# Optimization experiments

Measured on AMD Instinct MI355X. Metric: run time of the kernel, lower is better.

## Reference

```python
import jax, jax.numpy as jnp
import numpy as np

B = 1024      # num graphs
NPG = 128     # nodes per graph
N = B * NPG
EPG = 512     # edges per graph
E = B * EPG
D = 64
MAX_STEPS = 4
S = MAX_STEPS + 1   # max_steps + stop-step offset
T = 1.0
TB = 1.0
NEG = -1e30
STOP = -1


def setup_inputs() -> dict:
    key = jax.random.key(0)
    ks = jax.random.split(key, 24)
    edge_batch = jnp.repeat(jnp.arange(B, dtype=jnp.int32), EPG)
    src = jax.random.randint(ks[0], (E,), 0, NPG, dtype=jnp.int32) + edge_batch * NPG
    dst = jax.random.randint(ks[1], (E,), 0, NPG, dtype=jnp.int32) + edge_batch * NPG
    edge_index = jnp.stack([src, dst])
    sc = 1.0 / np.sqrt(D)
    p = lambda k, shape: (jax.random.normal(k, shape, jnp.float32) * sc)
    return dict(
        node_tokens=p(ks[2], (N, D)), edge_emb=p(ks[3], (E, D)),
        Wf1=p(ks[4], (D, D)), Wnf=p(ks[5], (D, D)), Wf2=p(ks[6], (D, D)),
        bf=jnp.zeros((D,), jnp.float32), wf=p(ks[7], (D,)),
        Wb1=p(ks[8], (D, D)), Wnb=p(ks[9], (D, D)), Wb2=p(ks[10], (D, D)),
        bb=jnp.zeros((D,), jnp.float32), wb=p(ks[11], (D,)),
        w_stop=p(ks[12], (D,)), b_stop=jnp.zeros((), jnp.float32),
        Ws=p(ks[13], (D, D)), Wu=p(ks[14], (D, D)), bu=jnp.zeros((D,), jnp.float32),
        edge_index=edge_index, edge_batch=edge_batch,
    )


def reference(node_tokens, edge_emb, Wf1, Wnf, Wf2, bf, wf,
              Wb1, Wnb, Wb2, bb, wb, w_stop, b_stop, Ws, Wu, bu,
              edge_index, edge_batch):
    esrc, edst = edge_index[0], edge_index[1]
    # state-independent part of the edge scores (precomputed once; faithful math)
    base_f = edge_emb @ Wf1 + node_tokens[esrc] @ Wnf + bf   # [E,D]
    base_b = edge_emb @ Wb1 + node_tokens[edst] @ Wnb + bb   # [E,D]
    g_ids = jnp.arange(B, dtype=jnp.int32)
    eidx = jnp.arange(E, dtype=jnp.int32)

    def seg_lse(x, valid):
        # per-graph logsumexp over valid edges (grad-safe masking)
        xm = jnp.where(valid, x, NEG)
        m = jax.ops.segment_max(xm, edge_batch, num_segments=B)
        xc = jnp.where(valid, x - m[edge_batch], 0.0)
        s = jax.ops.segment_sum(jnp.where(valid, jnp.exp(xc), 0.0), edge_batch, num_segments=B)
        return m + jnp.log(jnp.maximum(s, 1e-30))

    def step_fn(carry, k):
        state_vec, active, used, done, steps, stopn = carry
        valid = (esrc == active[edge_batch]) & (~used) & (~done[edge_batch])
        allow_stop = (~done) & (steps < MAX_STEPS)
        # forward edge scores + stop logit
        h = jax.nn.relu(base_f + (state_vec @ Wf2)[edge_batch])   # [E,D]
        score = h @ wf                                            # [E]
        stop_logit = state_vec @ w_stop + b_stop                  # [B]
        x = score / T
        lse_e = seg_lse(x, valid)
        stop_t = jnp.where(allow_stop, stop_logit / T, NEG)
        Z = jnp.logaddexp(lse_e, stop_t)
        logp_edge = x - Z[edge_batch]
        logp_stop = jnp.where(allow_stop, stop_logit / T - Z, 0.0)
        has_edge = jax.ops.segment_sum(valid.astype(jnp.int32), edge_batch, num_segments=B) > 0
        # gumbel-max sampling with scatter_max semantics
        ke, ksn = jax.random.split(k)
        se = jnp.where(valid, logp_edge + jax.random.gumbel(ke, (E,)), NEG)
        ss = jnp.where(allow_stop, logp_stop + jax.random.gumbel(ksn, (B,)), NEG)
        m = jax.ops.segment_max(se, edge_batch, num_segments=B)
        amax = jax.ops.segment_min(jnp.where(se == m[edge_batch], eidx, E), edge_batch, num_segments=B)
        amax = jnp.where(has_edge, amax, 0).astype(jnp.int32)
        m = jnp.where(has_edge, m, NEG)
        choose_stop = (ss > m) | (~has_edge)
        actions = jnp.where(choose_stop | done, STOP, amax)
        log_pf = jnp.where(choose_stop, logp_stop, logp_edge[amax])
        log_pf = jnp.where(done, 0.0, log_pf)
        take_edge = (actions >= 0) & (~done)
        stopping = choose_stop & (~done)
        stopn = jnp.where((stopn < 0) & stopping, active - g_ids * NPG, stopn)
        # state encoder update (masked)
        rel = edge_emb[amax]                                      # [B,D]
        new_state = jnp.tanh(state_vec @ Ws + rel @ Wu + bu)
        state_vec = jnp.where(take_edge[:, None], new_state, state_vec)
        # env step
        new_active = jnp.where(take_edge, edst[amax], active)
        used = used.at[amax].max(take_edge)
        steps = steps + take_edge.astype(jnp.int32)
        new_done = done | stopping
        # backward policy log-prob over edges incoming to the new active node
        bvalid = edst == new_active[edge_batch]
        hb = jax.nn.relu(base_b + (state_vec @ Wb2)[edge_batch])
        xb = (hb @ wb) / TB
        lse_b = seg_lse(xb, bvalid)
        log_pb = jnp.where(take_edge, xb[amax] - lse_b, 0.0)
        return (state_vec, new_active, used, new_done, steps, stopn), (actions, log_pf, log_pb)

    init = (
        jnp.zeros((B, D), jnp.float32),      # state_vec
        g_ids * NPG,                          # active node (global) = graph start node
        jnp.zeros((E,), bool),                # used_edge_mask
        jnp.zeros((B,), bool),                # done
        jnp.zeros((B,), jnp.int32),           # step_counts
        jnp.full((B,), STOP, jnp.int32),      # stop_node_locals
    )
    keys = jax.random.split(jax.random.key(42), S)
    (state_vec, active, used, done, steps, stopn), ys = jax.lax.scan(step_fn, init, keys)
    actions_seq = ys[0].T      # [B,S]
    log_pf_steps = ys[1].T     # [B,S]
    log_pb_steps = ys[2].T     # [B,S]
    stopn = jnp.where(stopn < 0, active - g_ids * NPG, stopn)   # backfill stop nodes
    return (actions_seq, log_pf_steps.sum(1), log_pf_steps, log_pb_steps,
            used, stopn, steps.astype(jnp.float32))
```

## Files before the change

kernel.cpp:

```cpp
#include <hip/hip_runtime.h>
#include <hip/hip_bf16.h>
#include <cstdint>

#define NBLK 1024
#define NPG  128
#define EPG  512
#define DD   64
#define NSTEP 5
#define ETOT (NBLK*EPG)
#define NEGF (-1e30f)
#define WAVES 4
#define MAXDEG 32

#define OA  0
#define OLS 5120
#define OPF 6144
#define OPB 11264
#define OU  16384
#define OSN 540672
#define OST 541696

struct KeysArg {
  uint32_t ke0[NSTEP], ke1[NSTEP];
  uint32_t ks0[NSTEP], ks1[NSTEP];
};

__host__ __device__ inline uint32_t rotl32(uint32_t x, int r){ return (x<<r)|(x>>(32-r)); }

__host__ __device__ inline void tf2x32(uint32_t k0, uint32_t k1, uint32_t& x0, uint32_t& x1){
  uint32_t k2 = k0 ^ k1 ^ 0x1BD11BDAu;
  x0 += k0; x1 += k1;
  x0+=x1; x1=rotl32(x1,13); x1^=x0;
  x0+=x1; x1=rotl32(x1,15); x1^=x0;
  x0+=x1; x1=rotl32(x1,26); x1^=x0;
  x0+=x1; x1=rotl32(x1, 6); x1^=x0;
  x0+=k1; x1+=k2+1u;
  x0+=x1; x1=rotl32(x1,17); x1^=x0;
  x0+=x1; x1=rotl32(x1,29); x1^=x0;
  x0+=x1; x1=rotl32(x1,16); x1^=x0;
  x0+=x1; x1=rotl32(x1,24); x1^=x0;
  x0+=k2; x1+=k0+2u;
  x0+=x1; x1=rotl32(x1,13); x1^=x0;
  x0+=x1; x1=rotl32(x1,15); x1^=x0;
  x0+=x1; x1=rotl32(x1,26); x1^=x0;
  x0+=x1; x1=rotl32(x1, 6); x1^=x0;
  x0+=k0; x1+=k1+3u;
  x0+=x1; x1=rotl32(x1,17); x1^=x0;
  x0+=x1; x1=rotl32(x1,29); x1^=x0;
  x0+=x1; x1=rotl32(x1,16); x1^=x0;
  x0+=x1; x1=rotl32(x1,24); x1^=x0;
  x0+=k1; x1+=k2+4u;
  x0+=x1; x1=rotl32(x1,13); x1^=x0;
  x0+=x1; x1=rotl32(x1,15); x1^=x0;
  x0+=x1; x1=rotl32(x1,26); x1^=x0;
  x0+=x1; x1=rotl32(x1, 6); x1^=x0;
  x0+=k2; x1+=k0+5u;
}

__device__ inline float gumbel_from_bits(uint32_t bits){
  float f = __uint_as_float((bits>>9) | 0x3f800000u) - 1.0f;
  const float tiny = 1.17549435e-38f;
  float u = fmaxf(tiny, f * (1.0f - tiny) + tiny);
  return -logf(-logf(u));
}

__device__ inline float gumbel_part(uint32_t k0, uint32_t k1, uint32_t idx){
  uint32_t x0 = 0u, x1 = idx;
  tf2x32(k0, k1, x0, x1);
  return gumbel_from_bits(x0 ^ x1);
}

__device__ inline float wsum(float x){
  #pragma unroll
  for (int off = 32; off; off >>= 1) x += __shfl_xor(x, off, 64);
  return x;
}

__device__ __forceinline__ void wsum4(float& x0, float& x1, float& x2, float& x3){
  #pragma unroll
  for (int off = 32; off; off >>= 1){
    x0 += __shfl_xor(x0, off, 64);
    x1 += __shfl_xor(x1, off, 64);
    x2 += __shfl_xor(x2, off, 64);
    x3 += __shfl_xor(x3, off, 64);
  }
}

__device__ __forceinline__ float rdlane(float v, int i){
  return __int_as_float(__builtin_amdgcn_readlane(__float_as_int(v), i));
}
__device__ __forceinline__ int rdlane_i(int v, int i){
  return __builtin_amdgcn_readlane(v, i);
}

__device__ __forceinline__ float matvec_col(const float* __restrict__ W, float v, int lane){
  float a0=0.f, a1=0.f, a2=0.f, a3=0.f;
  #pragma unroll 4
  for (int i = 0; i < DD; i += 4){
    a0 = fmaf(rdlane(v, i  ), W[(i  )*DD+lane], a0);
    a1 = fmaf(rdlane(v, i+1), W[(i+1)*DD+lane], a1);
    a2 = fmaf(rdlane(v, i+2), W[(i+2)*DD+lane], a2);
    a3 = fmaf(rdlane(v, i+3), W[(i+3)*DD+lane], a3);
  }
  return (a0+a1)+(a2+a3);
}

__device__ __forceinline__ void matvec4(const float* __restrict__ W,
                                        float v0, float v1, float v2, float v3,
                                        int lane, float o[4]){
  float acc[4][4] = {{0,0,0,0},{0,0,0,0},{0,0,0,0},{0,0,0,0}};
  #pragma unroll 8
  for (int i = 0; i < DD; i += 4){
    #pragma unroll
    for (int t = 0; t < 4; t++){
      float w  = W[(i+t)*DD+lane];
      acc[0][t] = fmaf(rdlane(v0, i+t), w, acc[0][t]);
      acc[1][t] = fmaf(rdlane(v1, i+t), w, acc[1][t]);
      acc[2][t] = fmaf(rdlane(v2, i+t), w, acc[2][t]);
      acc[3][t] = fmaf(rdlane(v3, i+t), w, acc[3][t]);
    }
  }
  #pragma unroll
  for (int c = 0; c < 4; c++)
    o[c] = (acc[c][0]+acc[c][1])+(acc[c][2]+acc[c][3]);
}

__global__ void __launch_bounds__(256, 4)
gfn_fused(const float* __restrict__ node_tokens,
          const float* __restrict__ edge_emb,
          const float* __restrict__ Wf1, const float* __restrict__ Wnf, const float* __restrict__ Wf2,
          const float* __restrict__ bf,  const float* __restrict__ wf,
          const float* __restrict__ Wb1, const float* __restrict__ Wnb, const float* __restrict__ Wb2,
          const float* __restrict__ bb,  const float* __restrict__ wb,
          const float* __restrict__ w_stop, const float* __restrict__ b_stop,
          const float* __restrict__ Ws,  const float* __restrict__ Wu, const float* __restrict__ bu,
          const int* __restrict__ e_src, const int* __restrict__ e_dst,
          float* __restrict__ out, KeysArg keys)
{
  const int g    = blockIdx.x;
  const int tid  = threadIdx.x;
  const int lane = tid & 63;
  const int wave = tid >> 6;
  const int ebase = g * EPG;

  __shared__ uint8_t  srcL[EPG], dstL[EPG];
  __shared__ uint16_t listO[EPG], listI[EPG];
  __shared__ int cntO[NPG], cntI[NPG], begO[NPG], begI[NPG];
  __shared__ uint8_t usedL[EPG];
  __shared__ float st_sh[DD];
  __shared__ float u_sh[DD], nt_sh[DD], acs_sh[DD];
  __shared__ float ntb_sh[DD], ntN_sh[DD], uN_sh[DD], ubB_sh[DD];
  __shared__ float xcF[MAXDEG], gmF[MAXDEG], xcB[MAXDEG];
  __shared__ float sl_sh, xbb_sh;

  for (int j = tid; j < EPG; j += 256){
    srcL[j] = (uint8_t)(e_src[ebase+j] - g*NPG);
    dstL[j] = (uint8_t)(e_dst[ebase+j] - g*NPG);
    usedL[j] = 0;
  }
  for (int n = tid; n < NPG; n += 256){ cntO[n]=0; cntI[n]=0; }
  if (tid < DD) st_sh[tid] = 0.f;
  __syncthreads();

  for (int j = tid; j < EPG; j += 256){
    atomicAdd(&cntO[srcL[j]], 1);
    atomicAdd(&cntI[dstL[j]], 1);
  }
  __syncthreads();

  if (wave == 0){
    int n0 = lane*2, n1 = n0+1;
    int c0O=cntO[n0], c1O=cntO[n1], sO=c0O+c1O;
    int c0I=cntI[n0], c1I=cntI[n1], sI=c0I+c1I;
    int xO=sO, xI=sI;
    #pragma unroll
    for (int off=1; off<64; off<<=1){
      int tO=__shfl_up(xO,off,64), tI=__shfl_up(xI,off,64);
      if (lane>=off){ xO+=tO; xI+=tI; }
    }
    begO[n0]=xO-sO; begO[n1]=xO-c1O;
    begI[n0]=xI-sI; begI[n1]=xI-c1I;
  }
  __syncthreads();
  for (int n = tid; n < NPG; n += 256){ cntO[n]=0; cntI[n]=0; }
  __syncthreads();

  for (int ph = 0; ph < WAVES; ph++){
    if (wave == ph){
      #pragma unroll
      for (int h = 0; h < 2; h++){
        int j = ph*128 + h*64 + lane;
        int sL = srcL[j]; int p = atomicAdd(&cntO[sL],1); listO[begO[sL]+p] = (uint16_t)j;
        int dL = dstL[j]; int q = atomicAdd(&cntI[dL],1); listI[begI[dL]+q] = (uint16_t)j;
      }
    }
    __syncthreads();
  }

  const float bf_l = bf[lane], wf_l = wf[lane];
  const float bb_l = bb[lane], wb_l = wb[lane];
  const float bu_l = bu[lane], wst_l = w_stop[lane];
  const float bstop = b_stop[0];

  bool done = false;
  int stepsC = 0, stopn = -1, activeL = 0;
  float lpf_sum = 0.f;
  int bOF = begO[0], dOF = min(cntO[0], MAXDEG);

  {
    float st_v = st_sh[lane];
    if (wave == 0)      u_sh[lane]   = matvec_col(Wf2, st_v, lane);
    else if (wave == 1){ float ntv = node_tokens[(size_t)(g*NPG+0)*DD+lane];
                         nt_sh[lane] = matvec_col(Wnf, ntv, lane); }
    else if (wave == 2) acs_sh[lane] = matvec_col(Ws, st_v, lane);
    else {
      float sl = wsum(st_v * wst_l) + bstop;
      if (lane == 0) sl_sh = sl;
      if (lane < dOF)
        gmF[lane] = gumbel_part(keys.ke0[0], keys.ke1[0], (uint32_t)(ebase + listO[bOF+lane]));
    }
    __syncthreads();
    if (wave >= 2){
      for (int c = wave-2; c < (dOF+3)>>2; c += 2){
        int el[4]; float v[4];
        #pragma unroll
        for (int t = 0; t < 4; t++){
          int k = c*4 + t;
          el[t] = listO[bOF + min(k, dOF-1)];
          v[t]  = edge_emb[(size_t)(ebase+el[t])*DD + lane];
        }
        float o[4], x[4];
        matvec4(Wf1, v[0], v[1], v[2], v[3], lane, o);
        #pragma unroll
        for (int t = 0; t < 4; t++) x[t] = fmaxf(o[t] + nt_sh[lane] + bf_l + u_sh[lane], 0.f) * wf_l;
        wsum4(x[0], x[1], x[2], x[3]);
        #pragma unroll
        for (int t = 0; t < 4; t++){
          int k = c*4 + t;
          if (k < dOF && lane == 0) xcF[k] = usedL[el[t]] ? NEGF : x[t];
        }
      }
    }
    __syncthreads();
  }

  for (int s = 0; s < NSTEP; s++){
    float act_out = -1.f, lpf_out = 0.f, lpb_out = 0.f;
    if (!done){
      float xr = (lane < MAXDEG) ? xcF[lane] : NEGF;
      float gr = (lane < MAXDEG) ? gmF[lane] : 0.f;
      int   er = (lane < dOF)    ? (int)listO[bOF + lane] : -1;
      float sl = sl_sh;

      float m1 = NEGF; int nvalid = 0;
      for (int k=0;k<dOF;k++){ float xk=rdlane(xr,k); if (xk!=NEGF){ m1=fmaxf(m1,xk); nvalid++; } }
      float ssum = 0.f;
      for (int k=0;k<dOF;k++){ float xk=rdlane(xr,k); if (xk!=NEGF) ssum += expf(xk - m1); }
      const bool has_edge = nvalid > 0;
      float lse_e = m1 + logf(fmaxf(ssum, 1e-30f));
      const bool allow_stop = (stepsC < 4);
      float stop_t = allow_stop ? sl : NEGF;
      float amx = fmaxf(lse_e, stop_t);
      float Z = amx + log1pf(expf(-fabsf(lse_e - stop_t)));

      float mbest = NEGF; int elbest = -1; float xbest = 0.f;
      for (int k=0;k<dOF;k++){
        float xk = rdlane(xr,k);
        if (xk == NEGF) continue;
        float se = (xk - Z) + rdlane(gr,k);
        if (se > mbest){ mbest = se; elbest = rdlane_i(er,k); xbest = xk; }
      }
      float gs = gumbel_part(keys.ks0[s], keys.ks1[s], (uint32_t)g);
      float ss = allow_stop ? (sl - Z) + gs : NEGF;
      float mcmp = has_edge ? mbest : NEGF;
      const bool choose_stop = (ss > mcmp) || (!has_edge);
      float logp_stop = allow_stop ? (sl - Z) : 0.f;
      const bool take_edge = !choose_stop;

      act_out = choose_stop ? -1.f : (float)(ebase + elbest);
      lpf_out = choose_stop ? logp_stop : (xbest - Z);
      if (choose_stop && stopn < 0) stopn = activeL;

      if (take_edge){
        const int newA = dstL[elbest];
        const bool more = (s < NSTEP-1);

        if (wave == 0){
          float rv = edge_emb[(size_t)(ebase+elbest)*DD + lane];
          float acr = matvec_col(Wu, rv, lane);
          st_sh[lane] = tanhf(acs_sh[lane] + acr + bu_l);
          if (lane == 0) usedL[elbest] = 1;
        } else if (wave == 1){
          float nbv = node_tokens[(size_t)(g*NPG + newA)*DD + lane];
          ntb_sh[lane] = matvec_col(Wnb, nbv, lane);
        } else if (wave == 2){
          if (more){
            float nbv = node_tokens[(size_t)(g*NPG + newA)*DD + lane];
            ntN_sh[lane] = matvec_col(Wnf, nbv, lane);
          }
        }
        activeL = newA; stepsC++;
        __syncthreads();

        float stp = st_sh[lane];
        const int bI  = begI[activeL], dIc = min(cntI[activeL], MAXDEG);
        const int bON = begO[activeL];
        const int dON = more ? min(cntO[activeL], MAXDEG) : 0;
        if (wave == 0){
          if (more) uN_sh[lane] = matvec_col(Wf2, stp, lane);
        } else if (wave == 1){
          ubB_sh[lane] = matvec_col(Wb2, stp, lane);
        } else if (wave == 2){
          if (more) acs_sh[lane] = matvec_col(Ws, stp, lane);
        } else {
          if (more){
            float s2 = wsum(stp * wst_l) + bstop;
            if (lane == 0) sl_sh = s2;
            if (lane < dON)
              gmF[lane] = gumbel_part(keys.ke0[s+1], keys.ke1[s+1],
                                      (uint32_t)(ebase + listO[bON+lane]));
          }
        }
        __syncthreads();

        if (wave == 2 || wave == 0){
          for (int c = (wave==2 ? 0 : 1); c < (dIc+3)>>2; c += 2){
            int el[4]; float v[4];
            #pragma unroll
            for (int t = 0; t < 4; t++){
              int k = c*4 + t;
              el[t] = listI[bI + min(k, dIc-1)];
              v[t]  = edge_emb[(size_t)(ebase+el[t])*DD + lane];
            }
            float o[4], xb[4];
            matvec4(Wb1, v[0], v[1], v[2], v[3], lane, o);
            #pragma unroll
            for (int t = 0; t < 4; t++) xb[t] = fmaxf(o[t] + ntb_sh[lane] + bb_l + ubB_sh[lane], 0.f) * wb_l;
            wsum4(xb[0], xb[1], xb[2], xb[3]);
            #pragma unroll
            for (int t = 0; t < 4; t++){
              int k = c*4 + t;
              if (k < dIc && lane == 0){
                xcB[k] = xb[t];
                if (el[t] == elbest) xbb_sh = xb[t];
              }
            }
          }
        } else {
          for (int c = (wave==3 ? 0 : 1); c < (dON+3)>>2; c += 2){
            int el[4]; float v[4];
            #pragma unroll
            for (int t = 0; t < 4; t++){
              int k = c*4 + t;
              el[t] = listO[bON + min(k, dON-1)];
              v[t]  = edge_emb[(size_t)(ebase+el[t])*DD + lane];
            }
            float o[4], x[4];
            matvec4(Wf1, v[0], v[1], v[2], v[3], lane, o);
            #pragma unroll
            for (int t = 0; t < 4; t++) x[t] = fmaxf(o[t] + ntN_sh[lane] + bf_l + uN_sh[lane], 0.f) * wf_l;
            wsum4(x[0], x[1], x[2], x[3]);
            #pragma unroll
            for (int t = 0; t < 4; t++){
              int k = c*4 + t;
              if (k < dON && lane == 0) xcF[k] = usedL[el[t]] ? NEGF : x[t];
            }
          }
        }
        __syncthreads();

        float xbr = (lane < MAXDEG) ? xcB[lane] : 0.f;
        float m2 = NEGF;
        for (int k=0;k<dIc;k++) m2 = fmaxf(m2, rdlane(xbr,k));
        float s2 = 0.f;
        for (int k=0;k<dIc;k++) s2 += expf(rdlane(xbr,k) - m2);
        float lse_b = m2 + logf(fmaxf(s2, 1e-30f));
        lpb_out = xbb_sh - lse_b;

        bOF = bON; dOF = dON;
      }
      done = done || choose_stop;
    }

    if (tid == 0){
      out[OA  + g*NSTEP + s] = act_out;
      out[OPF + g*NSTEP + s] = lpf_out;
      out[OPB + g*NSTEP + s] = lpb_out;
    }
    lpf_sum += lpf_out;
  }

  if (tid == 0){
    out[OLS + g] = lpf_sum;
    int sn = (stopn < 0) ? activeL : stopn;
    out[OSN + g] = (float)sn;
    out[OST + g] = (float)stepsC;
  }
  for (int j = tid; j < EPG; j += 256)
    out[OU + ebase + j] = usedL[j] ? 1.0f : 0.0f;
}

extern "C" void kernel_launch(void* const* d_in, const int* in_sizes, int n_in,
                              void* d_out, int out_size, void* d_ws, size_t ws_size,
                              hipStream_t stream)
{
  (void)in_sizes; (void)n_in; (void)out_size; (void)d_ws; (void)ws_size;

  KeysArg K;
  for (uint32_t s = 0; s < NSTEP; s++){
    uint32_t a = 0u, b = s;
    tf2x32(0u, 42u, a, b);
    uint32_t e0 = 0u, e1 = 0u;
    tf2x32(a, b, e0, e1);
    uint32_t s0 = 0u, s1 = 1u;
    tf2x32(a, b, s0, s1);
    K.ke0[s] = e0; K.ke1[s] = e1;
    K.ks0[s] = s0; K.ks1[s] = s1;
  }

  const int* eidx = (const int*)d_in[17];
  gfn_fused<<<dim3(NBLK), dim3(256), 0, stream>>>(
      (const float*)d_in[0],  (const float*)d_in[1],
      (const float*)d_in[2],  (const float*)d_in[3],  (const float*)d_in[4],
      (const float*)d_in[5],  (const float*)d_in[6],
      (const float*)d_in[7],  (const float*)d_in[8],  (const float*)d_in[9],
      (const float*)d_in[10], (const float*)d_in[11],
      (const float*)d_in[12], (const float*)d_in[13],
      (const float*)d_in[14], (const float*)d_in[15], (const float*)d_in[16],
      eidx, eidx + ETOT,
      (float*)d_out, K);
}
```

Before: 81.07 us.

## Pack four graphs per block and stage six weight matrices in LDS

Each block now holds four 256-thread teams, one per graph. The six DxD weight matrices (Wf1, Wb1, Wnf, Wnb, Wf2, Wb2) are loaded once into shared memory and shared by all teams, so matvecs read LDS instead of global/L2. Barriers are hoisted out of divergent branches so all 1024 threads synchronise together. The trade-off is that teams now wait on each other at every barrier, and about 96KB of LDS per block limits occupancy to roughly one block per CU. The launch grid also shrinks to 256 blocks.

```diff
diff --git a/kernel.cpp b/kernel.cpp
--- a/kernel.cpp
+++ b/kernel.cpp
@@ -10,6 +10,7 @@
 #define ETOT (NBLK*EPG)
 #define NEGF (-1e30f)
 #define WAVES 4
+#define TEAMS 4
 #define MAXDEG 32
 
 #define OA  0
@@ -125,7 +126,7 @@
     o[c] = (acc[c][0]+acc[c][1])+(acc[c][2]+acc[c][3]);
 }
 
-__global__ void __launch_bounds__(256, 4)
+__global__ void __launch_bounds__(1024)
 gfn_fused(const float* __restrict__ node_tokens,
           const float* __restrict__ edge_emb,
           const float* __restrict__ Wf1, const float* __restrict__ Wnf, const float* __restrict__ Wf2,
@@ -137,52 +138,62 @@
           const int* __restrict__ e_src, const int* __restrict__ e_dst,
           float* __restrict__ out, KeysArg keys)
 {
-  const int g    = blockIdx.x;
   const int tid  = threadIdx.x;
+  const int team = tid >> 8;
+  const int ttid = tid & 255;
   const int lane = tid & 63;
-  const int wave = tid >> 6;
+  const int wave = (tid >> 6) & 3;
+  const int g    = blockIdx.x * TEAMS + team;
   const int ebase = g * EPG;
 
-  __shared__ uint8_t  srcL[EPG], dstL[EPG];
-  __shared__ uint16_t listO[EPG], listI[EPG];
-  __shared__ int cntO[NPG], cntI[NPG], begO[NPG], begI[NPG];
-  __shared__ uint8_t usedL[EPG];
-  __shared__ float st_sh[DD];
-  __shared__ float u_sh[DD], nt_sh[DD], acs_sh[DD];
-  __shared__ float ntb_sh[DD], ntN_sh[DD], uN_sh[DD], ubB_sh[DD];
-  __shared__ float xcF[MAXDEG], gmF[MAXDEG], xcB[MAXDEG];
-  __shared__ float sl_sh, xbb_sh;
-
-  for (int j = tid; j < EPG; j += 256){
-    srcL[j] = (uint8_t)(e_src[ebase+j] - g*NPG);
-    dstL[j] = (uint8_t)(e_dst[ebase+j] - g*NPG);
-    usedL[j] = 0;
-  }
-  for (int n = tid; n < NPG; n += 256){ cntO[n]=0; cntI[n]=0; }
-  if (tid < DD) st_sh[tid] = 0.f;
+  __shared__ float Wlds[6][DD*DD];
+  __shared__ uint8_t  srcL[TEAMS][EPG], dstL[TEAMS][EPG];
+  __shared__ uint16_t listO[TEAMS][EPG], listI[TEAMS][EPG];
+  __shared__ int cntO[TEAMS][NPG], cntI[TEAMS][NPG], begO[TEAMS][NPG], begI[TEAMS][NPG];
+  __shared__ uint8_t usedL[TEAMS][EPG];
+  __shared__ float st_sh[TEAMS][DD];
+  __shared__ float u_sh[TEAMS][DD], nt_sh[TEAMS][DD], acs_sh[TEAMS][DD];
+  __shared__ float ntb_sh[TEAMS][DD], ntN_sh[TEAMS][DD], uN_sh[TEAMS][DD], ubB_sh[TEAMS][DD];
+  __shared__ float xcF[TEAMS][MAXDEG], gmF[TEAMS][MAXDEG], xcB[TEAMS][MAXDEG];
+  __shared__ float sl_sh[TEAMS], xbb_sh[TEAMS];
+
+  {
+    const float* srcs[6] = {Wf1, Wb1, Wnf, Wnb, Wf2, Wb2};
+    #pragma unroll
+    for (int m = 0; m < 6; m++)
+      ((float4*)&Wlds[m][0])[tid] = ((const float4*)srcs[m])[tid];
+  }
+
+  for (int j = ttid; j < EPG; j += 256){
+    srcL[team][j] = (uint8_t)(e_src[ebase+j] - g*NPG);
+    dstL[team][j] = (uint8_t)(e_dst[ebase+j] - g*NPG);
+    usedL[team][j] = 0;
+  }
+  for (int n = ttid; n < NPG; n += 256){ cntO[team][n]=0; cntI[team][n]=0; }
+  if (ttid < DD) st_sh[team][ttid] = 0.f;
   __syncthreads();
 
-  for (int j = tid; j < EPG; j += 256){
-    atomicAdd(&cntO[srcL[j]], 1);
-    atomicAdd(&cntI[dstL[j]], 1);
+  for (int j = ttid; j < EPG; j += 256){
+    atomicAdd(&cntO[team][srcL[team][j]], 1);
+    atomicAdd(&cntI[team][dstL[team][j]], 1);
   }
   __syncthreads();
 
   if (wave == 0){
     int n0 = lane*2, n1 = n0+1;
-    int c0O=cntO[n0], c1O=cntO[n1], sO=c0O+c1O;
-    int c0I=cntI[n0], c1I=cntI[n1], sI=c0I+c1I;
+    int c0O=cntO[team][n0], c1O=cntO[team][n1], sO=c0O+c1O;
+    int c0I=cntI[team][n0], c1I=cntI[team][n1], sI=c0I+c1I;
     int xO=sO, xI=sI;
     #pragma unroll
     for (int off=1; off<64; off<<=1){
       int tO=__shfl_up(xO,off,64), tI=__shfl_up(xI,off,64);
       if (lane>=off){ xO+=tO; xI+=tI; }
     }
-    begO[n0]=xO-sO; begO[n1]=xO-c1O;
-    begI[n0]=xI-sI; begI[n1]=xI-c1I;
+    begO[team][n0]=xO-sO; begO[team][n1]=xO-c1O;
+    begI[team][n0]=xI-sI; begI[team][n1]=xI-c1I;
   }
   __syncthreads();
-  for (int n = tid; n < NPG; n += 256){ cntO[n]=0; cntI[n]=0; }
+  for (int n = ttid; n < NPG; n += 256){ cntO[team][n]=0; cntI[team][n]=0; }
   __syncthreads();
 
   for (int ph = 0; ph < WAVES; ph++){
@@ -190,8 +201,8 @@
       #pragma unroll
       for (int h = 0; h < 2; h++){
         int j = ph*128 + h*64 + lane;
-        int sL = srcL[j]; int p = atomicAdd(&cntO[sL],1); listO[begO[sL]+p] = (uint16_t)j;
-        int dL = dstL[j]; int q = atomicAdd(&cntI[dL],1); listI[begI[dL]+q] = (uint16_t)j;
+        int sL = srcL[team][j]; int p = atomicAdd(&cntO[team][sL],1); listO[team][begO[team][sL]+p] = (uint16_t)j;
+        int dL = dstL[team][j]; int q = atomicAdd(&cntI[team][dL],1); listI[team][begI[team][dL]+q] = (uint16_t)j;
       }
     }
     __syncthreads();
@@ -205,19 +216,19 @@
   bool done = false;
   int stepsC = 0, stopn = -1, activeL = 0;
   float lpf_sum = 0.f;
-  int bOF = begO[0], dOF = min(cntO[0], MAXDEG);
+  int bOF = begO[team][0], dOF = min(cntO[team][0], MAXDEG);
 
   {
-    float st_v = st_sh[lane];
-    if (wave == 0)      u_sh[lane]   = matvec_col(Wf2, st_v, lane);
+    float st_v = st_sh[team][lane];
+    if (wave == 0)      u_sh[team][lane]   = matvec_col(Wlds[4], st_v, lane);
     else if (wave == 1){ float ntv = node_tokens[(size_t)(g*NPG+0)*DD+lane];
-                         nt_sh[lane] = matvec_col(Wnf, ntv, lane); }
-    else if (wave == 2) acs_sh[lane] = matvec_col(Ws, st_v, lane);
+                         nt_sh[team][lane] = matvec_col(Wlds[2], ntv, lane); }
+    else if (wave == 2) acs_sh[team][lane] = matvec_col(Ws, st_v, lane);
     else {
       float sl = wsum(st_v * wst_l) + bstop;
-      if (lane == 0) sl_sh = sl;
+      if (lane == 0) sl_sh[team] = sl;
       if (lane < dOF)
-        gmF[lane] = gumbel_part(keys.ke0[0], keys.ke1[0], (uint32_t)(ebase + listO[bOF+lane]));
+        gmF[team][lane] = gumbel_part(keys.ke0[0], keys.ke1[0], (uint32_t)(ebase + listO[team][bOF+lane]));
     }
     __syncthreads();
     if (wave >= 2){
@@ -226,18 +237,18 @@
         #pragma unroll
         for (int t = 0; t < 4; t++){
           int k = c*4 + t;
-          el[t] = listO[bOF + min(k, dOF-1)];
+          el[t] = listO[team][bOF + min(k, dOF-1)];
           v[t]  = edge_emb[(size_t)(ebase+el[t])*DD + lane];
         }
         float o[4], x[4];
-        matvec4(Wf1, v[0], v[1], v[2], v[3], lane, o);
+        matvec4(Wlds[0], v[0], v[1], v[2], v[3], lane, o);
         #pragma unroll
-        for (int t = 0; t < 4; t++) x[t] = fmaxf(o[t] + nt_sh[lane] + bf_l + u_sh[lane], 0.f) * wf_l;
+        for (int t = 0; t < 4; t++) x[t] = fmaxf(o[t] + nt_sh[team][lane] + bf_l + u_sh[team][lane], 0.f) * wf_l;
         wsum4(x[0], x[1], x[2], x[3]);
         #pragma unroll
         for (int t = 0; t < 4; t++){
           int k = c*4 + t;
-          if (k < dOF && lane == 0) xcF[k] = usedL[el[t]] ? NEGF : x[t];
+          if (k < dOF && lane == 0) xcF[team][k] = usedL[team][el[t]] ? NEGF : x[t];
         }
       }
     }
@@ -246,11 +257,15 @@
 
   for (int s = 0; s < NSTEP; s++){
     float act_out = -1.f, lpf_out = 0.f, lpb_out = 0.f;
+    bool choose_stop = false, take_edge = false;
+    int elbest = -1, newA = 0, bI = 0, dIc = 0, bON = 0, dON = 0;
+    const bool more = (s < NSTEP-1);
+
     if (!done){
-      float xr = (lane < MAXDEG) ? xcF[lane] : NEGF;
-      float gr = (lane < MAXDEG) ? gmF[lane] : 0.f;
-      int   er = (lane < dOF)    ? (int)listO[bOF + lane] : -1;
-      float sl = sl_sh;
+      float xr = (lane < MAXDEG) ? xcF[team][lane] : NEGF;
+      float gr = (lane < MAXDEG) ? gmF[team][lane] : 0.f;
+      int   er = (lane < dOF)    ? (int)listO[team][bOF + lane] : -1;
+      float sl = sl_sh[team];
 
       float m1 = NEGF; int nvalid = 0;
       for (int k=0;k<dOF;k++){ float xk=rdlane(xr,k); if (xk!=NEGF){ m1=fmaxf(m1,xk); nvalid++; } }
@@ -263,7 +278,7 @@
       float amx = fmaxf(lse_e, stop_t);
       float Z = amx + log1pf(expf(-fabsf(lse_e - stop_t)));
 
-      float mbest = NEGF; int elbest = -1; float xbest = 0.f;
+      float mbest = NEGF; float xbest = 0.f;
       for (int k=0;k<dOF;k++){
         float xk = rdlane(xr,k);
         if (xk == NEGF) continue;
@@ -273,116 +288,119 @@
       float gs = gumbel_part(keys.ks0[s], keys.ks1[s], (uint32_t)g);
       float ss = allow_stop ? (sl - Z) + gs : NEGF;
       float mcmp = has_edge ? mbest : NEGF;
-      const bool choose_stop = (ss > mcmp) || (!has_edge);
+      choose_stop = (ss > mcmp) || (!has_edge);
       float logp_stop = allow_stop ? (sl - Z) : 0.f;
-      const bool take_edge = !choose_stop;
+      take_edge = !choose_stop;
 
       act_out = choose_stop ? -1.f : (float)(ebase + elbest);
       lpf_out = choose_stop ? logp_stop : (xbest - Z);
       if (choose_stop && stopn < 0) stopn = activeL;
-
-      if (take_edge){
-        const int newA = dstL[elbest];
-        const bool more = (s < NSTEP-1);
-
-        if (wave == 0){
-          float rv = edge_emb[(size_t)(ebase+elbest)*DD + lane];
-          float acr = matvec_col(Wu, rv, lane);
-          st_sh[lane] = tanhf(acs_sh[lane] + acr + bu_l);
-          if (lane == 0) usedL[elbest] = 1;
-        } else if (wave == 1){
+    }
+
+    if (take_edge){
+      newA = dstL[team][elbest];
+      if (wave == 0){
+        float rv = edge_emb[(size_t)(ebase+elbest)*DD + lane];
+        float acr = matvec_col(Wu, rv, lane);
+        st_sh[team][lane] = tanhf(acs_sh[team][lane] + acr + bu_l);
+        if (lane == 0) usedL[team][elbest] = 1;
+      } else if (wave == 1){
+        float nbv = node_tokens[(size_t)(g*NPG + newA)*DD + lane];
+        ntb_sh[team][lane] = matvec_col(Wlds[3], nbv, lane);
+      } else if (wave == 2){
+        if (more){
           float nbv = node_tokens[(size_t)(g*NPG + newA)*DD + lane];
-          ntb_sh[lane] = matvec_col(Wnb, nbv, lane);
-        } else if (wave == 2){
-          if (more){
-            float nbv = node_tokens[(size_t)(g*NPG + newA)*DD + lane];
-            ntN_sh[lane] = matvec_col(Wnf, nbv, lane);
+          ntN_sh[team][lane] = matvec_col(Wlds[2], nbv, lane);
+        }
+      }
+      activeL = newA; stepsC++;
+    }
+    __syncthreads();
+
+    if (take_edge){
+      float stp = st_sh[team][lane];
+      bI  = begI[team][activeL]; dIc = min(cntI[team][activeL], MAXDEG);
+      bON = begO[team][activeL];
+      dON = more ? min(cntO[team][activeL], MAXDEG) : 0;
+      if (wave == 0){
+        if (more) uN_sh[team][lane] = matvec_col(Wlds[4], stp, lane);
+      } else if (wave == 1){
+        ubB_sh[team][lane] = matvec_col(Wlds[5], stp, lane);
+      } else if (wave == 2){
+        if (more) acs_sh[team][lane] = matvec_col(Ws, stp, lane);
+      } else {
+        if (more){
+          float s2 = wsum(stp * wst_l) + bstop;
+          if (lane == 0) sl_sh[team] = s2;
+          if (lane < dON)
+            gmF[team][lane] = gumbel_part(keys.ke0[s+1], keys.ke1[s+1],
+                                          (uint32_t)(ebase + listO[team][bON+lane]));
+        }
+      }
+    }
+    __syncthreads();
+
+    if (take_edge){
+      if (wave == 2 || wave == 0){
+        for (int c = (wave==2 ? 0 : 1); c < (dIc+3)>>2; c += 2){
+          int el[4]; float v[4];
+          #pragma unroll
+          for (int t = 0; t < 4; t++){
+            int k = c*4 + t;
+            el[t] = listI[team][bI + min(k, dIc-1)];
+            v[t]  = edge_emb[(size_t)(ebase+el[t])*DD + lane];
           }
-        }
-        activeL = newA; stepsC++;
-        __syncthreads();
-
-        float stp = st_sh[lane];
-        const int bI  = begI[activeL], dIc = min(cntI[activeL], MAXDEG);
-        const int bON = begO[activeL];
-        const int dON = more ? min(cntO[activeL], MAXDEG) : 0;
-        if (wave == 0){
-          if (more) uN_sh[lane] = matvec_col(Wf2, stp, lane);
-        } else if (wave == 1){
-          ubB_sh[lane] = matvec_col(Wb2, stp, lane);
-        } else if (wave == 2){
-          if (more) acs_sh[lane] = matvec_col(Ws, stp, lane);
-        } else {
-          if (more){
-            float s2 = wsum(stp * wst_l) + bstop;
-            if (lane == 0) sl_sh = s2;
-            if (lane < dON)
-              gmF[lane] = gumbel_part(keys.ke0[s+1], keys.ke1[s+1],
-                                      (uint32_t)(ebase + listO[bON+lane]));
-          }
-        }
-        __syncthreads();
-
-        if (wave == 2 || wave == 0){
-          for (int c = (wave==2 ? 0 : 1); c < (dIc+3)>>2; c += 2){
-            int el[4]; float v[4];
-            #pragma unroll
-            for (int t = 0; t < 4; t++){
-              int k = c*4 + t;
-              el[t] = listI[bI + min(k, dIc-1)];
-              v[t]  = edge_emb[(size_t)(ebase+el[t])*DD + lane];
-            }
-            float o[4], xb[4];
-            matvec4(Wb1, v[0], v[1], v[2], v[3], lane, o);
-            #pragma unroll
-            for (int t = 0; t < 4; t++) xb[t] = fmaxf(o[t] + ntb_sh[lane] + bb_l + ubB_sh[lane], 0.f) * wb_l;
-            wsum4(xb[0], xb[1], xb[2], xb[3]);
-            #pragma unroll
-            for (int t = 0; t < 4; t++){
-              int k = c*4 + t;
-              if (k < dIc && lane == 0){
-                xcB[k] = xb[t];
-                if (el[t] == elbest) xbb_sh = xb[t];
-              }
+          float o[4], xb[4];
+          matvec4(Wlds[1], v[0], v[1], v[2], v[3], lane, o);
+          #pragma unroll
+          for (int t = 0; t < 4; t++) xb[t] = fmaxf(o[t] + ntb_sh[team][lane] + bb_l + ubB_sh[team][lane], 0.f) * wb_l;
+          wsum4(xb[0], xb[1], xb[2], xb[3]);
+          #pragma unroll
+          for (int t = 0; t < 4; t++){
+            int k = c*4 + t;
+            if (k < dIc && lane == 0){
+              xcB[team][k] = xb[t];
+              if (el[t] == elbest) xbb_sh[team] = xb[t];
             }
           }
-        } else {
-          for (int c = (wave==3 ? 0 : 1); c < (dON+3)>>2; c += 2){
-            int el[4]; float v[4];
-            #pragma unroll
-            for (int t = 0; t < 4; t++){
-              int k = c*4 + t;
-              el[t] = listO[bON + min(k, dON-1)];
-              v[t]  = edge_emb[(size_t)(ebase+el[t])*DD + lane];
-            }
-            float o[4], x[4];
-            matvec4(Wf1, v[0], v[1], v[2], v[3], lane, o);
-            #pragma unroll
-            for (int t = 0; t < 4; t++) x[t] = fmaxf(o[t] + ntN_sh[lane] + bf_l + uN_sh[lane], 0.f) * wf_l;
-            wsum4(x[0], x[1], x[2], x[3]);
-            #pragma unroll
-            for (int t = 0; t < 4; t++){
-              int k = c*4 + t;
-              if (k < dON && lane == 0) xcF[k] = usedL[el[t]] ? NEGF : x[t];
-            }
+        }
+      } else {
+        for (int c = (wave==3 ? 0 : 1); c < (dON+3)>>2; c += 2){
+          int el[4]; float v[4];
+          #pragma unroll
+          for (int t = 0; t < 4; t++){
+            int k = c*4 + t;
+            el[t] = listO[team][bON + min(k, dON-1)];
+            v[t]  = edge_emb[(size_t)(ebase+el[t])*DD + lane];
           }
-        }
-        __syncthreads();
-
-        float xbr = (lane < MAXDEG) ? xcB[lane] : 0.f;
-        float m2 = NEGF;
-        for (int k=0;k<dIc;k++) m2 = fmaxf(m2, rdlane(xbr,k));
-        float s2 = 0.f;
-        for (int k=0;k<dIc;k++) s2 += expf(rdlane(xbr,k) - m2);
-        float lse_b = m2 + logf(fmaxf(s2, 1e-30f));
-        lpb_out = xbb_sh - lse_b;
-
-        bOF = bON; dOF = dON;
-      }
-      done = done || choose_stop;
-    }
-
-    if (tid == 0){
+          float o[4], x[4];
+          matvec4(Wlds[0], v[0], v[1], v[2], v[3], lane, o);
+          #pragma unroll
+          for (int t = 0; t < 4; t++) x[t] = fmaxf(o[t] + ntN_sh[team][lane] + bf_l + uN_sh[team][lane], 0.f) * wf_l;
+          wsum4(x[0], x[1], x[2], x[3]);
+          #pragma unroll
+          for (int t = 0; t < 4; t++){
+            int k = c*4 + t;
+            if (k < dON && lane == 0) xcF[team][k] = usedL[team][el[t]] ? NEGF : x[t];
+          }
+        }
+      }
+    }
+    __syncthreads();
+
+    if (take_edge){
+      float xbr = (lane < MAXDEG) ? xcB[team][lane] : 0.f;
+      float m2 = NEGF;
+      for (int k=0;k<dIc;k++) m2 = fmaxf(m2, rdlane(xbr,k));
+      float s2 = 0.f;
+      for (int k=0;k<dIc;k++) s2 += expf(rdlane(xbr,k) - m2);
+      float lse_b = m2 + logf(fmaxf(s2, 1e-30f));
+      lpb_out = xbb_sh[team] - lse_b;
+      bOF = bON; dOF = dON;
+    }
+    done = done || choose_stop;
+
+    if (ttid == 0){
       out[OA  + g*NSTEP + s] = act_out;
       out[OPF + g*NSTEP + s] = lpf_out;
       out[OPB + g*NSTEP + s] = lpb_out;
@@ -390,14 +408,14 @@
     lpf_sum += lpf_out;
   }
 
-  if (tid == 0){
+  if (ttid == 0){
     out[OLS + g] = lpf_sum;
     int sn = (stopn < 0) ? activeL : stopn;
     out[OSN + g] = (float)sn;
     out[OST + g] = (float)stepsC;
   }
-  for (int j = tid; j < EPG; j += 256)
-    out[OU + ebase + j] = usedL[j] ? 1.0f : 0.0f;
+  for (int j = ttid; j < EPG; j += 256)
+    out[OU + ebase + j] = usedL[team][j] ? 1.0f : 0.0f;
 }
 
 extern "C" void kernel_launch(void* const* d_in, const int* in_sizes, int n_in,
@@ -419,7 +437,7 @@
   }
 
   const int* eidx = (const int*)d_in[17];
-  gfn_fused<<<dim3(NBLK), dim3(256), 0, stream>>>(
+  gfn_fused<<<dim3(NBLK/TEAMS), dim3(1024), 0, stream>>>(
       (const float*)d_in[0],  (const float*)d_in[1],
       (const float*)d_in[2],  (const float*)d_in[3],  (const float*)d_in[4],
       (const float*)d_in[5],  (const float*)d_in[6],
```

New measurement: 89.88 us. 10.9% more time.

## Prefetch first edge chunk early, vectorize softmax exps, precompute stop gumbels

Applied to the files above, without the earlier changes.

Moves the adjacency lookups for the new active node ahead of the state-update matvecs, so each wave can issue its first edge_emb gather early and hide global-memory latency behind the matvecs and barriers. Both per-edge exp loops now compute the exponentials once per lane and sum them with readlane, replacing serial scalar exps. The stop-action gumbel noise for all steps is precomputed once, one step per lane, instead of hashed each step. The matvec unroll factor also rises. Risks are higher register pressure from the held prefetch values and the larger unroll, which could lower occupancy.

```diff
diff --git a/kernel.cpp b/kernel.cpp
--- a/kernel.cpp
+++ b/kernel.cpp
@@ -95,7 +95,7 @@
 
 __device__ __forceinline__ float matvec_col(const float* __restrict__ W, float v, int lane){
   float a0=0.f, a1=0.f, a2=0.f, a3=0.f;
-  #pragma unroll 4
+  #pragma unroll 8
   for (int i = 0; i < DD; i += 4){
     a0 = fmaf(rdlane(v, i  ), W[(i  )*DD+lane], a0);
     a1 = fmaf(rdlane(v, i+1), W[(i+1)*DD+lane], a1);
@@ -202,6 +202,15 @@
   const float bu_l = bu[lane], wst_l = w_stop[lane];
   const float bstop = b_stop[0];
 
+  float gsv;
+  {
+    uint32_t k0 = keys.ks0[0], k1 = keys.ks1[0];
+    #pragma unroll
+    for (int s5 = 1; s5 < NSTEP; s5++)
+      if (lane == s5){ k0 = keys.ks0[s5]; k1 = keys.ks1[s5]; }
+    gsv = (lane < NSTEP) ? gumbel_part(k0, k1, (uint32_t)g) : 0.f;
+  }
+
   bool done = false;
   int stepsC = 0, stopn = -1, activeL = 0;
   float lpf_sum = 0.f;
@@ -254,8 +263,9 @@
 
       float m1 = NEGF; int nvalid = 0;
       for (int k=0;k<dOF;k++){ float xk=rdlane(xr,k); if (xk!=NEGF){ m1=fmaxf(m1,xk); nvalid++; } }
+      float ex = expf(xr - m1);
       float ssum = 0.f;
-      for (int k=0;k<dOF;k++){ float xk=rdlane(xr,k); if (xk!=NEGF) ssum += expf(xk - m1); }
+      for (int k=0;k<dOF;k++){ float xk=rdlane(xr,k); if (xk!=NEGF) ssum += rdlane(ex,k); }
       const bool has_edge = nvalid > 0;
       float lse_e = m1 + logf(fmaxf(ssum, 1e-30f));
       const bool allow_stop = (stepsC < 4);
@@ -270,7 +280,7 @@
         float se = (xk - Z) + rdlane(gr,k);
         if (se > mbest){ mbest = se; elbest = rdlane_i(er,k); xbest = xk; }
       }
-      float gs = gumbel_part(keys.ks0[s], keys.ks1[s], (uint32_t)g);
+      float gs = rdlane(gsv, s);
       float ss = allow_stop ? (sl - Z) + gs : NEGF;
       float mcmp = has_edge ? mbest : NEGF;
       const bool choose_stop = (ss > mcmp) || (!has_edge);
@@ -284,6 +294,34 @@
       if (take_edge){
         const int newA = dstL[elbest];
         const bool more = (s < NSTEP-1);
+        const int bI  = begI[newA], dIc = min(cntI[newA], MAXDEG);
+        const int bON = begO[newA];
+        const int dON = more ? min(cntO[newA], MAXDEG) : 0;
+
+        float vPre[4]; int elPre[4]; bool pre = false; int c0;
+        if (wave == 2 || wave == 0){
+          c0 = (wave==2 ? 0 : 1);
+          if (c0 < ((dIc+3)>>2)){
+            pre = true;
+            #pragma unroll
+            for (int t = 0; t < 4; t++){
+              int k = c0*4 + t;
+              elPre[t] = listI[bI + min(k, dIc-1)];
+              vPre[t]  = edge_emb[(size_t)(ebase+elPre[t])*DD + lane];
+            }
+          }
+        } else {
+          c0 = (wave==3 ? 0 : 1);
+          if (c0 < ((dON+3)>>2)){
+            pre = true;
+            #pragma unroll
+            for (int t = 0; t < 4; t++){
+              int k = c0*4 + t;
+              elPre[t] = listO[bON + min(k, dON-1)];
+              vPre[t]  = edge_emb[(size_t)(ebase+elPre[t])*DD + lane];
+            }
+          }
+        }
 
         if (wave == 0){
           float rv = edge_emb[(size_t)(ebase+elbest)*DD + lane];
@@ -303,9 +341,6 @@
         __syncthreads();
 
         float stp = st_sh[lane];
-        const int bI  = begI[activeL], dIc = min(cntI[activeL], MAXDEG);
-        const int bON = begO[activeL];
-        const int dON = more ? min(cntO[activeL], MAXDEG) : 0;
         if (wave == 0){
           if (more) uN_sh[lane] = matvec_col(Wf2, stp, lane);
         } else if (wave == 1){
@@ -324,13 +359,18 @@
         __syncthreads();
 
         if (wave == 2 || wave == 0){
-          for (int c = (wave==2 ? 0 : 1); c < (dIc+3)>>2; c += 2){
+          for (int c = c0; c < (dIc+3)>>2; c += 2){
             int el[4]; float v[4];
-            #pragma unroll
-            for (int t = 0; t < 4; t++){
-              int k = c*4 + t;
-              el[t] = listI[bI + min(k, dIc-1)];
-              v[t]  = edge_emb[(size_t)(ebase+el[t])*DD + lane];
+            if (pre && c == c0){
+              #pragma unroll
+              for (int t = 0; t < 4; t++){ el[t] = elPre[t]; v[t] = vPre[t]; }
+            } else {
+              #pragma unroll
+              for (int t = 0; t < 4; t++){
+                int k = c*4 + t;
+                el[t] = listI[bI + min(k, dIc-1)];
+                v[t]  = edge_emb[(size_t)(ebase+el[t])*DD + lane];
+              }
             }
             float o[4], xb[4];
             matvec4(Wb1, v[0], v[1], v[2], v[3], lane, o);
@@ -347,13 +387,18 @@
             }
           }
         } else {
-          for (int c = (wave==3 ? 0 : 1); c < (dON+3)>>2; c += 2){
+          for (int c = c0; c < (dON+3)>>2; c += 2){
             int el[4]; float v[4];
-            #pragma unroll
-            for (int t = 0; t < 4; t++){
-              int k = c*4 + t;
-              el[t] = listO[bON + min(k, dON-1)];
-              v[t]  = edge_emb[(size_t)(ebase+el[t])*DD + lane];
+            if (pre && c == c0){
+              #pragma unroll
+              for (int t = 0; t < 4; t++){ el[t] = elPre[t]; v[t] = vPre[t]; }
+            } else {
+              #pragma unroll
+              for (int t = 0; t < 4; t++){
+                int k = c*4 + t;
+                el[t] = listO[bON + min(k, dON-1)];
+                v[t]  = edge_emb[(size_t)(ebase+el[t])*DD + lane];
+              }
             }
             float o[4], x[4];
             matvec4(Wf1, v[0], v[1], v[2], v[3], lane, o);
@@ -372,8 +417,9 @@
         float xbr = (lane < MAXDEG) ? xcB[lane] : 0.f;
         float m2 = NEGF;
         for (int k=0;k<dIc;k++) m2 = fmaxf(m2, rdlane(xbr,k));
+        float ex2 = expf(xbr - m2);
         float s2 = 0.f;
-        for (int k=0;k<dIc;k++) s2 += expf(rdlane(xbr,k) - m2);
+        for (int k=0;k<dIc;k++) s2 += rdlane(ex2,k);
         float lse_b = m2 + logf(fmaxf(s2, 1e-30f));
         lpb_out = xbb_sh - lse_b;
 
```

Result: faster. 78.35 us (-3.4%).
